# Kernel tuning notes

Measured on AMD Instinct MI355X. Metric: run time of the kernel, lower is better.

## Reference

```python
import jax, jax.numpy as jnp
import numpy as np

B, S, C = 32, 512, 384
MAX_LEN = 4096
MAX_DUR = 16


def setup_inputs() -> dict:
    key = jax.random.key(0)
    kx, kd = jax.random.split(key)
    x = jax.random.normal(kx, (B, S, C), dtype=jnp.float32)
    durations = jax.random.randint(kd, (B, S), 0, MAX_DUR, dtype=jnp.int32)
    return {"x": x, "durations": durations, "max_length": MAX_LEN}


def reference(x, durations, max_length):
    # Round (no-op for int durations, kept for faithfulness to torch.round().long())
    d = jnp.round(durations.astype(jnp.float32)).astype(jnp.int32)  # [B, S]
    # _limit_durations is equivalent to clipping the cumulative sum at max_length:
    # the first token crossing max_length gets truncated, all later tokens zeroed.
    ends = jnp.clip(jnp.cumsum(d, axis=1), 0, max_length)          # [B, S]
    total = ends[:, -1]                                            # [B]
    t = jnp.arange(max_length, dtype=jnp.int32)                    # [T]
    # frame t belongs to phoneme j where starts[j] <= t < ends[j];
    # searchsorted(ends, t, 'right') skips zero-duration tokens automatically.
    idx = jax.vmap(lambda e: jnp.searchsorted(e, t, side='right'))(ends)  # [B, T]
    mel_masks = t[None, :] >= total[:, None]                       # [B, T] True = pad
    idx_c = jnp.clip(idx, 0, x.shape[1] - 1)
    expanded = jnp.take_along_axis(x, idx_c[:, :, None], axis=1)   # [B, T, C]
    expanded = jnp.where(mel_masks[:, :, None], jnp.zeros((), x.dtype), expanded)
    return expanded, mel_masks
```

## Files before the change

kernel.cpp:

```cpp
#include <hip/hip_runtime.h>

#define BATCH 32
#define SEQ 512
#define CH 384
#define CH4 96
#define MAXL 4096
#define ZBLK 64

typedef float v4f __attribute__((ext_vector_type(4)));

__global__ __launch_bounds__(SEQ) void lr_scan_kernel(
    const int* __restrict__ durations,
    const int* __restrict__ max_len_p,
    int* __restrict__ ws_ends,
    float* __restrict__ out_mask)
{
    __shared__ int s_cum[SEQ];

    const int tid = threadIdx.x;
    const int b = blockIdx.x;
    const int maxlen = max_len_p[0];

    s_cum[tid] = durations[b * SEQ + tid];
    __syncthreads();
    #pragma unroll
    for (int off = 1; off < SEQ; off <<= 1) {
        int v = (tid >= off) ? s_cum[tid - off] : 0;
        __syncthreads();
        s_cum[tid] += v;
        __syncthreads();
    }

    ws_ends[b * SEQ + tid] = min(s_cum[tid], maxlen);
    const int total = min(s_cum[SEQ - 1], maxlen);

    #pragma unroll
    for (int t = tid; t < MAXL; t += SEQ)
        out_mask[b * MAXL + t] = (t >= total) ? 1.0f : 0.0f;
}

__global__ __launch_bounds__(128) void lr_scatter_kernel(
    const v4f* __restrict__ x,
    const int* __restrict__ ws_ends,
    v4f* __restrict__ out)
{
    const int tid = threadIdx.x;
    const int bid = blockIdx.x;

    if (bid < BATCH * SEQ) {
        const int b = bid >> 9;
        const int j = bid & (SEQ - 1);
        const int e  = ws_ends[bid];
        const int st = j ? ws_ends[bid - 1] : 0;
        if (tid >= CH4 || e <= st) return;
        v4f v = x[(size_t)bid * CH4 + tid];
        v4f* ob = out + ((size_t)(b << 12) + st) * CH4 + tid;
        for (int t = st; t < e; ++t) {
            *ob = v;
            ob += CH4;
        }
    } else {
        const int z = bid - BATCH * SEQ;
        const int b = z >> 6;
        const int i = z & (ZBLK - 1);
        const int total = ws_ends[b * SEQ + SEQ - 1];
        if (tid >= CH4) return;
        const v4f zero = (v4f){0.f, 0.f, 0.f, 0.f};
        for (int t = total + i; t < MAXL; t += ZBLK)
            out[((size_t)(b << 12) + t) * CH4 + tid] = zero;
    }
}

extern "C" void kernel_launch(void* const* d_in, const int* in_sizes, int n_in,
                              void* d_out, int out_size, void* d_ws, size_t ws_size,
                              hipStream_t stream) {
    const v4f* x = (const v4f*)d_in[0];
    const int* durations = (const int*)d_in[1];
    const int* max_len_p = (const int*)d_in[2];
    float* out = (float*)d_out;
    float* out_mask = out + (size_t)BATCH * MAXL * CH;
    int* ws_ends = (int*)d_ws;

    lr_scan_kernel<<<BATCH, SEQ, 0, stream>>>(durations, max_len_p, ws_ends, out_mask);
    lr_scatter_kernel<<<BATCH * SEQ + BATCH * ZBLK, 128, 0, stream>>>(
        x, ws_ends, (v4f*)out);
}
```

Baseline: 218.8 us.

## Fuse duration scan into scatter kernel with per-block wave-shuffle prefix sum

Removes the separate scan kernel and the workspace round-trip by having every block recompute the per-batch cumulative durations with vectorized loads and a 64-lane shuffle scan into shared memory. Mask writes are folded into the frame and padding blocks. This saves a launch and global ends traffic, at the cost of redundant scan work per block and an extra barrier.

Result: no change. 216.2 us (-1.2%).

```diff
diff --git a/kernel.cpp b/kernel.cpp
--- a/kernel.cpp
+++ b/kernel.cpp
@@ -2,72 +2,79 @@
 
 #define BATCH 32
 #define SEQ 512
-#define CH 384
 #define CH4 96
 #define MAXL 4096
 #define ZBLK 64
+#define FBLKS (BATCH * SEQ)
+#define THREADS 128
 
 typedef float v4f __attribute__((ext_vector_type(4)));
+typedef int   v4i __attribute__((ext_vector_type(4)));
 
-__global__ __launch_bounds__(SEQ) void lr_scan_kernel(
-    const int* __restrict__ durations,
+__global__ __launch_bounds__(THREADS) void lr_fused(
+    const v4f* __restrict__ x,
+    const v4i* __restrict__ dur4,
     const int* __restrict__ max_len_p,
-    int* __restrict__ ws_ends,
+    v4f* __restrict__ out,
     float* __restrict__ out_mask)
 {
-    __shared__ int s_cum[SEQ];
+    __shared__ int s_end[SEQ];
 
     const int tid = threadIdx.x;
-    const int b = blockIdx.x;
-    const int maxlen = max_len_p[0];
+    const int bid = blockIdx.x;
+    const bool is_frame = (bid < FBLKS);
+    const int b = is_frame ? (bid >> 9) : ((bid - FBLKS) >> 6);
 
-    s_cum[tid] = durations[b * SEQ + tid];
+    if (tid < 64) {
+        const v4i* dp = dur4 + b * (SEQ / 4) + tid * 2;
+        v4i d0 = dp[0], d1 = dp[1];
+        int lane_sum = d0.x + d0.y + d0.z + d0.w + d1.x + d1.y + d1.z + d1.w;
+        int incl = lane_sum;
+        #pragma unroll
+        for (int off = 1; off < 64; off <<= 1) {
+            int v = __shfl_up(incl, off, 64);
+            if (tid >= off) incl += v;
+        }
+        int cum = incl - lane_sum;
+        const int maxlen = max_len_p[0];
+        const int base = tid * 8;
+        cum += d0.x; s_end[base + 0] = min(cum, maxlen);
+        cum += d0.y; s_end[base + 1] = min(cum, maxlen);
+        cum += d0.z; s_end[base + 2] = min(cum, maxlen);
+        cum += d0.w; s_end[base + 3] = min(cum, maxlen);
+        cum += d1.x; s_end[base + 4] = min(cum, maxlen);
+        cum += d1.y; s_end[base + 5] = min(cum, maxlen);
+        cum += d1.z; s_end[base + 6] = min(cum, maxlen);
+        cum += d1.w; s_end[base + 7] = min(cum, maxlen);
+    }
     __syncthreads();
-    #pragma unroll
-    for (int off = 1; off < SEQ; off <<= 1) {
-        int v = (tid >= off) ? s_cum[tid - off] : 0;
-        __syncthreads();
-        s_cum[tid] += v;
-        __syncthreads();
-    }
 
-    ws_ends[b * SEQ + tid] = min(s_cum[tid], maxlen);
-    const int total = min(s_cum[SEQ - 1], maxlen);
-
-    #pragma unroll
-    for (int t = tid; t < MAXL; t += SEQ)
-        out_mask[b * MAXL + t] = (t >= total) ? 1.0f : 0.0f;
-}
-
-__global__ __launch_bounds__(128) void lr_scatter_kernel(
-    const v4f* __restrict__ x,
-    const int* __restrict__ ws_ends,
-    v4f* __restrict__ out)
-{
-    const int tid = threadIdx.x;
-    const int bid = blockIdx.x;
-
-    if (bid < BATCH * SEQ) {
-        const int b = bid >> 9;
-        const int j = bid & (SEQ - 1);
-        const int e  = ws_ends[bid];
-        const int st = j ? ws_ends[bid - 1] : 0;
-        if (tid >= CH4 || e <= st) return;
-        v4f v = x[(size_t)bid * CH4 + tid];
-        v4f* ob = out + ((size_t)(b << 12) + st) * CH4 + tid;
-        for (int t = st; t < e; ++t) {
-            *ob = v;
-            ob += CH4;
+    if (is_frame) {
+        const int j  = bid & (SEQ - 1);
+        const int e  = s_end[j];
+        const int st = j ? s_end[j - 1] : 0;
+        const int n  = e - st;
+        if (n <= 0) return;
+        if (tid < n)
+            out_mask[(b << 12) + st + tid] = 0.0f;
+        if (tid < CH4) {
+            v4f v = x[(size_t)bid * CH4 + tid];
+            v4f* ob = out + ((size_t)(b << 12) + st) * CH4 + tid;
+            for (int k = 0; k < n; ++k) {
+                *ob = v;
+                ob += CH4;
+            }
         }
     } else {
-        const int z = bid - BATCH * SEQ;
-        const int b = z >> 6;
-        const int i = z & (ZBLK - 1);
-        const int total = ws_ends[b * SEQ + SEQ - 1];
-        if (tid >= CH4) return;
+        const int i = (bid - FBLKS) & (ZBLK - 1);
+        const int total = s_end[SEQ - 1];
         const v4f zero = (v4f){0.f, 0.f, 0.f, 0.f};
-        for (int t = total + i; t < MAXL; t += ZBLK)
-            out[((size_t)(b << 12) + t) * CH4 + tid] = zero;
+        for (int t = total + i; t < MAXL; t += ZBLK) {
+            if (tid < CH4)
+                out[((size_t)(b << 12) + t) * CH4 + tid] = zero;
+            else if (tid == CH4)
+                out_mask[(b << 12) + t] = 1.0f;
+        }
     }
 }
 
@@ -75,13 +82,11 @@
                               void* d_out, int out_size, void* d_ws, size_t ws_size,
                               hipStream_t stream) {
     const v4f* x = (const v4f*)d_in[0];
-    const int* durations = (const int*)d_in[1];
+    const v4i* dur4 = (const v4i*)d_in[1];
     const int* max_len_p = (const int*)d_in[2];
     float* out = (float*)d_out;
-    float* out_mask = out + (size_t)BATCH * MAXL * CH;
-    int* ws_ends = (int*)d_ws;
+    float* out_mask = out + (size_t)BATCH * MAXL * CH4 * 4;
 
-    lr_scan_kernel<<<BATCH, SEQ, 0, stream>>>(durations, max_len_p, ws_ends, out_mask);
-    lr_scatter_kernel<<<BATCH * SEQ + BATCH * ZBLK, 128, 0, stream>>>(
-        x, ws_ends, (v4f*)out);
+    lr_fused<<<FBLKS + BATCH * ZBLK, THREADS, 0, stream>>>(
+        x, dur4, max_len_p, (v4f*)out, out_mask);
 }
```
